# Kernel tuning notes

Measured on AMD Instinct MI355X. Metric: run time of the kernel, lower is better.

## Reference

```python
import jax, jax.numpy as jnp
import numpy as np

NUM_HEADS = 8
NUM_LEVELS = 4
NUM_POINTS = 4


def setup_inputs() -> dict:
    key = jax.random.key(0)
    kq, kp, kv, k1, k2, k3, k4 = jax.random.split(key, 7)
    B, Q, C = 4, 4096, 256
    M, L, P = NUM_HEADS, NUM_LEVELS, NUM_POINTS
    shapes_np = np.array([[128, 128], [64, 64], [32, 32], [16, 16]], dtype=np.int32)
    sizes = shapes_np[:, 0] * shapes_np[:, 1]
    N = int(sizes.sum())  # 21760
    level_index = jnp.asarray(np.concatenate([[0], np.cumsum(sizes)[:-1]]).astype(np.int32))
    q = jax.random.normal(kq, (B, Q, C), jnp.float32)
    p = jax.random.uniform(kp, (B, Q, L, 2), jnp.float32)  # normalized ref points
    v = jax.random.normal(kv, (B, N, C), jnp.float32)
    # proj_offset bias: radial grid init from reset_parameters()
    t = np.arange(M, dtype=np.float32) * (2.0 * np.pi / M)
    grid = np.stack([np.cos(t), np.sin(t)], -1)
    grid = grid / np.abs(grid).max(-1, keepdims=True)
    grid = np.tile(grid[:, None, None, :], (1, L, P, 1)) * np.arange(1, P + 1, dtype=np.float32)[None, None, :, None]
    b_off = jnp.asarray(grid.reshape(-1))
    s = 1.0 / np.sqrt(C).astype(np.float32)
    W_off = jax.random.normal(k1, (C, M * L * P * 2), jnp.float32) * 0.01
    W_attn = jax.random.normal(k2, (C, M * L * P), jnp.float32) * s
    b_attn = jnp.zeros((M * L * P,), jnp.float32)
    W_val = jax.random.normal(k3, (C, C), jnp.float32) * s
    b_val = jnp.zeros((C,), jnp.float32)
    W_out = jax.random.normal(k4, (C, C), jnp.float32) * s
    b_out = jnp.zeros((C,), jnp.float32)
    return {"q": q, "p": p, "v": v, "shapes": jnp.asarray(shapes_np), "level_index": level_index,
            "W_off": W_off, "b_off": b_off, "W_attn": W_attn, "b_attn": b_attn,
            "W_val": W_val, "b_val": b_val, "W_out": W_out, "b_out": b_out}


def _ms_deform_attn(q, p, v, shapes, level_index, W_off, b_off, W_attn, b_attn, W_val, b_val, W_out, b_out):
    B, Q, C = q.shape
    M, L, P = NUM_HEADS, NUM_LEVELS, NUM_POINTS
    D = C // M
    N = v.shape[1]
    # value projection -> [B, M, N, D] (head-major for gather)
    v_p = (v @ W_val + b_val).reshape(B, N, M, D).transpose(0, 2, 1, 3)
    # attention weights, softmax over L*P (classic MSDeformAttn kernel contract)
    attn = jax.nn.softmax((q @ W_attn + b_attn).reshape(B, Q, M, L * P), axis=-1)
    attn = attn.reshape(B, Q, M, L, P)
    # sampling locations (P==2 reference-point branch)
    off = (q @ W_off + b_off).reshape(B, Q, M, L, P, 2)
    norm = jnp.stack([shapes[:, 1], shapes[:, 0]], -1).astype(jnp.float32)  # (W, H) per level
    loc = p[:, :, None, :, None, :] + off / norm[None, None, None, :, None, :]  # [B,Q,M,L,P,2]

    out = jnp.zeros((B, M, Q, D), jnp.float32)
    for l in range(L):
        Hf = shapes[l, 0].astype(jnp.float32)
        Wf = shapes[l, 1].astype(jnp.float32)
        Hi = shapes[l, 0]
        Wi = shapes[l, 1]
        base = level_index[l]
        # grid_sample(align_corners=False) convention: pixel = loc*size - 0.5
        x = loc[:, :, :, l, :, 0] * Wf - 0.5  # [B,Q,M,P]
        y = loc[:, :, :, l, :, 1] * Hf - 0.5
        x0 = jnp.floor(x)
        y0 = jnp.floor(y)
        lx, ly = x - x0, y - y0
        x0i = x0.astype(jnp.int32)
        y0i = y0.astype(jnp.int32)

        def corner(xi, yi, w):
            valid = (xi >= 0) & (xi < Wi) & (yi >= 0) & (yi < Hi)
            idx = base + jnp.clip(yi, 0, Hi - 1) * Wi + jnp.clip(xi, 0, Wi - 1)  # [B,Q,M,P]
            idx = idx.transpose(0, 2, 1, 3).reshape(B, M, Q * P)
            g = jnp.take_along_axis(v_p, idx[..., None], axis=2).reshape(B, M, Q, P, D)
            wv = (w * valid.astype(w.dtype)).transpose(0, 2, 1, 3)[..., None]  # [B,M,Q,P,1]
            return g * wv

        samp = (corner(x0i, y0i, (1 - lx) * (1 - ly))
                + corner(x0i + 1, y0i, lx * (1 - ly))
                + corner(x0i, y0i + 1, (1 - lx) * ly)
                + corner(x0i + 1, y0i + 1, lx * ly))  # [B,M,Q,P,D]
        a_l = attn[:, :, :, l, :].transpose(0, 2, 1, 3)  # [B,M,Q,P]
        out = out + jnp.einsum('bmqpd,bmqp->bmqd', samp, a_l)

    out = out.transpose(0, 2, 1, 3).reshape(B, Q, M * D)
    return out @ W_out + b_out


def reference(q, p, v, shapes, level_index, W_off, b_off, W_attn, b_attn, W_val, b_val, W_out, b_out):
    return _ms_deform_attn(q, p, v, shapes, level_index, W_off, b_off, W_attn, b_attn, W_val, b_val, W_out, b_out)
```

## Files before the change

kernel.cpp:

```cpp
#include <hip/hip_runtime.h>
#include <cstddef>

#define BB 4
#define QQ 4096
#define MM 8
#define NN 21760

typedef __bf16 bf16_8 __attribute__((ext_vector_type(8)));
typedef __bf16 bf16_4 __attribute__((ext_vector_type(4)));
typedef float  floatx4 __attribute__((ext_vector_type(4)));

__global__ __launch_bounds__(256) void prep_weights(
    const float* __restrict__ Wv, const float* __restrict__ Wa,
    const float* __restrict__ Wo, const float* __restrict__ Wu,
    const float* __restrict__ ba, const float* __restrict__ bo,
    __bf16* __restrict__ Wt, float* __restrict__ biasq)
{
    const int gid = blockIdx.x * 256 + threadIdx.x;
    if (gid < 65536) {
        const int n = gid >> 8, k = gid & 255;
        Wt[gid] = (__bf16)Wv[k * 256 + n];
    } else if (gid < 163840) {
        const int o = gid - 65536;
        const int n = o >> 8, k = o & 255;
        Wt[gid] = (__bf16)(n < 128 ? Wa[k * 128 + n] : Wo[k * 256 + (n - 128)]);
    } else if (gid < 229376) {
        const int o = gid - 163840;
        const int n = o >> 8, k = o & 255;
        Wt[gid] = (__bf16)Wu[k * 256 + n];
    } else if (gid < 229760) {
        const int j = gid - 229376;
        biasq[j] = (j < 128) ? ba[j] : bo[j - 128];
    }
}

__global__ __launch_bounds__(512, 4) void gemm_vq(
    const float* __restrict__ v,
    const float* __restrict__ q,
    const __bf16* __restrict__ Wt,
    const float* __restrict__ b_val,
    const float* __restrict__ biasq,
    __bf16* __restrict__ vpb,
    float* __restrict__ gqp)
{
    __shared__ __bf16 As[64][256];

    const int tid  = threadIdx.x;
    const int lane = tid & 63;
    const int wave = tid >> 6;
    const int quad = lane >> 4;
    const int l16  = lane & 15;
    const int flat = blockIdx.x;

    if (flat >= 768) {
        const int f2     = flat - 768;
        const int z      = f2 / 340;
        const int token0 = (f2 - z * 340) * 64;
        const float* Af  = v + (size_t)z * NN * 256;

        #pragma unroll
        for (int c = 0; c < 8; ++c) {
            const int cid = c * 512 + tid;
            const int r   = cid >> 6;
            const int kc  = (cid & 63) * 4;
            const float4 av = *(const float4*)(Af + (size_t)(token0 + r) * 256 + kc);
            bf16_4 w;
            w[0] = (__bf16)av.x; w[1] = (__bf16)av.y;
            w[2] = (__bf16)av.z; w[3] = (__bf16)av.w;
            const int col = ((((kc >> 3) ^ (r & 7)) << 3) | (kc & 7));
            *(bf16_4*)&As[r][col] = w;
        }

        bf16_8 wf[8][2];
        #pragma unroll
        for (int kk = 0; kk < 8; ++kk)
            #pragma unroll
            for (int j = 0; j < 2; ++j)
                wf[kk][j] = *(const bf16_8*)(Wt + (size_t)(wave * 32 + j * 16 + l16) * 256
                                              + kk * 32 + quad * 8);
        __syncthreads();

        floatx4 acc[2][4] = {};
        #pragma unroll
        for (int kk = 0; kk < 8; ++kk) {
            bf16_8 af[4];
            #pragma unroll
            for (int it = 0; it < 4; ++it)
                af[it] = *(const bf16_8*)&As[it * 16 + l16]
                                           [(((kk * 4 + quad) ^ (l16 & 7)) << 3)];
            #pragma unroll
            for (int j = 0; j < 2; ++j)
                #pragma unroll
                for (int it = 0; it < 4; ++it)
                    acc[j][it] = __builtin_amdgcn_mfma_f32_16x16x32_bf16(wf[kk][j], af[it], acc[j][it], 0, 0, 0);
        }

        #pragma unroll
        for (int j = 0; j < 2; ++j) {
            const int n0 = wave * 32 + j * 16 + quad * 4;
            const float4 b4 = *(const float4*)(b_val + n0);
            const int mh = n0 >> 5, dd = n0 & 31;
            #pragma unroll
            for (int it = 0; it < 4; ++it) {
                const int token = token0 + it * 16 + l16;
                bf16_4 ob;
                ob[0] = (__bf16)(acc[j][it][0] + b4.x);
                ob[1] = (__bf16)(acc[j][it][1] + b4.y);
                ob[2] = (__bf16)(acc[j][it][2] + b4.z);
                ob[3] = (__bf16)(acc[j][it][3] + b4.w);
                *(bf16_4*)(vpb + (((size_t)z * 8 + mh) * NN + token) * 32 + dd) = ob;
            }
        }
    } else {
        const int o      = flat;
        const int slice  = o >> 8;
        const int token0 = (o & 255) * 64;
        const int col0   = slice * 128;
        const __bf16* Wb = Wt + 65536 + (size_t)col0 * 256;

        #pragma unroll
        for (int c = 0; c < 8; ++c) {
            const int cid = c * 512 + tid;
            const int r   = cid >> 6;
            const int kc  = (cid & 63) * 4;
            const float4 av = *(const float4*)(q + (size_t)(token0 + r) * 256 + kc);
            bf16_4 w;
            w[0] = (__bf16)av.x; w[1] = (__bf16)av.y;
            w[2] = (__bf16)av.z; w[3] = (__bf16)av.w;
            const int col = ((((kc >> 3) ^ (r & 7)) << 3) | (kc & 7));
            *(bf16_4*)&As[r][col] = w;
        }

        bf16_8 wf[8];
        #pragma unroll
        for (int kk = 0; kk < 8; ++kk)
            wf[kk] = *(const bf16_8*)(Wb + (size_t)(wave * 16 + l16) * 256
                                       + kk * 32 + quad * 8);
        __syncthreads();

        floatx4 acc[4] = {};
        #pragma unroll
        for (int kk = 0; kk < 8; ++kk) {
            bf16_8 af[4];
            #pragma unroll
            for (int it = 0; it < 4; ++it)
                af[it] = *(const bf16_8*)&As[it * 16 + l16]
                                           [(((kk * 4 + quad) ^ (l16 & 7)) << 3)];
            #pragma unroll
            for (int it = 0; it < 4; ++it)
                acc[it] = __builtin_amdgcn_mfma_f32_16x16x32_bf16(wf[kk], af[it], acc[it], 0, 0, 0);
        }

        const int n0 = col0 + wave * 16 + quad * 4;
        const float4 b4 = *(const float4*)(biasq + n0);
        #pragma unroll
        for (int it = 0; it < 4; ++it) {
            const int token = token0 + it * 16 + l16;
            float4 ot;
            ot.x = acc[it][0] + b4.x;
            ot.y = acc[it][1] + b4.y;
            ot.z = acc[it][2] + b4.z;
            ot.w = acc[it][3] + b4.w;
            *(float4*)(gqp + (size_t)token * 384 + n0) = ot;
        }
    }
}

__device__ __forceinline__ float bflo(unsigned u) { return __uint_as_float(u << 16); }
__device__ __forceinline__ float bfhi(unsigned u) { return __uint_as_float(u & 0xffff0000u); }

__global__ __launch_bounds__(512) void sampler_out(
    const __bf16* __restrict__ vp,
    const float* __restrict__ gqp,
    const float* __restrict__ pref,
    const __bf16* __restrict__ Wout,
    const float* __restrict__ b_out,
    float* __restrict__ out)
{
    __shared__ __bf16 mids[16][256];

    const int t    = threadIdx.x;
    const int m    = t >> 6;
    const int lane = t & 63;
    const int s    = lane >> 2;
    const int c    = lane & 3;
    const int l    = s >> 2;
    const int bq0  = blockIdx.x * 16;

    const int   Hi = 128 >> l;
    const float Hf = (float)Hi;
    const int   base = (l == 0) ? 0 : (l == 1) ? 16384 : (l == 2) ? 20480 : 21504;
    const int b2 = (lane >> 2) & 1, b3 = (lane >> 3) & 1, b4i = (lane >> 4) & 1;

    for (int qi = 0; qi < 16; ++qi) {
        const int bq = bq0 + qi;
        const int b  = bq >> 12;

        const float logit = gqp[(size_t)bq * 384 + m * 16 + s];
        const float e = __expf(logit);
        float sum = e;
        #pragma unroll
        for (int k = 4; k < 64; k <<= 1) sum += __shfl_xor(sum, k, 64);
        const float a = e * __builtin_amdgcn_rcpf(sum);

        const float2 off = *(const float2*)(gqp + (size_t)bq * 384 + 128 + (m * 16 + s) * 2);
        const float2 pr  = *(const float2*)(pref + (size_t)bq * 8 + l * 2);

        const float x = fmaf(pr.x, Hf, off.x - 0.5f);
        const float y = fmaf(pr.y, Hf, off.y - 0.5f);
        const float x0f = floorf(x), y0f = floorf(y);
        const float lx = x - x0f, ly = y - y0f;
        const int x0 = (int)x0f, y0 = (int)y0f;
        const int cx0 = min(max(x0, 0), Hi - 1), cx1 = min(max(x0 + 1, 0), Hi - 1);
        const int cy0 = min(max(y0, 0), Hi - 1), cy1 = min(max(y0 + 1, 0), Hi - 1);
        const bool vx0 = (x0 >= 0) && (x0 < Hi), vx1 = (x0 + 1 >= 0) && (x0 + 1 < Hi);
        const bool vy0 = (y0 >= 0) && (y0 < Hi), vy1 = (y0 + 1 >= 0) && (y0 + 1 < Hi);
        const float w00 = a * (1.f - lx) * (1.f - ly) * ((vx0 && vy0) ? 1.f : 0.f);
        const float w10 = a * lx * (1.f - ly) * ((vx1 && vy0) ? 1.f : 0.f);
        const float w01 = a * (1.f - lx) * ly * ((vx0 && vy1) ? 1.f : 0.f);
        const float w11 = a * lx * ly * ((vx1 && vy1) ? 1.f : 0.f);

        const __bf16* vbase = vp + ((size_t)b * 8 + m) * NN * 32;
        const uint4 u00 = *((const uint4*)(vbase + (size_t)(base + cy0 * Hi + cx0) * 32) + c);
        const uint4 u10 = *((const uint4*)(vbase + (size_t)(base + cy0 * Hi + cx1) * 32) + c);
        const uint4 u01 = *((const uint4*)(vbase + (size_t)(base + cy1 * Hi + cx0) * 32) + c);
        const uint4 u11 = *((const uint4*)(vbase + (size_t)(base + cy1 * Hi + cx1) * 32) + c);

        float f[8];
        f[0] = w00*bflo(u00.x) + w10*bflo(u10.x) + w01*bflo(u01.x) + w11*bflo(u11.x);
        f[1] = w00*bfhi(u00.x) + w10*bfhi(u10.x) + w01*bfhi(u01.x) + w11*bfhi(u11.x);
        f[2] = w00*bflo(u00.y) + w10*bflo(u10.y) + w01*bflo(u01.y) + w11*bflo(u11.y);
        f[3] = w00*bfhi(u00.y) + w10*bfhi(u10.y) + w01*bfhi(u01.y) + w11*bfhi(u11.y);
        f[4] = w00*bflo(u00.z) + w10*bflo(u10.z) + w01*bflo(u01.z) + w11*bflo(u11.z);
        f[5] = w00*bfhi(u00.z) + w10*bfhi(u10.z) + w01*bfhi(u01.z) + w11*bfhi(u11.z);
        f[6] = w00*bflo(u00.w) + w10*bflo(u10.w) + w01*bflo(u01.w) + w11*bflo(u11.w);
        f[7] = w00*bfhi(u00.w) + w10*bfhi(u10.w) + w01*bfhi(u01.w) + w11*bfhi(u11.w);

        #pragma unroll
        for (int j = 0; j < 4; ++j) {
            const float sel  = b2 ? f[j] : f[j + 4];
            const float recv = __shfl_xor(sel, 4, 64);
            f[j] = (b2 ? f[j + 4] : f[j]) + recv;
        }
        #pragma unroll
        for (int j = 0; j < 2; ++j) {
            const float sel  = b3 ? f[j] : f[j + 2];
            const float recv = __shfl_xor(sel, 8, 64);
            f[j] = (b3 ? f[j + 2] : f[j]) + recv;
        }
        {
            const float sel  = b4i ? f[0] : f[1];
            const float recv = __shfl_xor(sel, 16, 64);
            f[0] = (b4i ? f[1] : f[0]) + recv;
        }
        f[0] += __shfl_xor(f[0], 32, 64);

        if (!(lane & 32)) {
            const int chan = (c << 3) | (b2 << 2) | (b3 << 1) | b4i;
            const int cf   = m * 32 + chan;
            const int p = ((((cf >> 3) ^ (qi & 7)) << 3) | (cf & 7));
            mids[qi][p] = (__bf16)f[0];
        }
    }
    __syncthreads();

    const int quad = lane >> 4;
    const int l16  = lane & 15;

    bf16_8 wf[8][2];
    #pragma unroll
    for (int kk = 0; kk < 8; ++kk)
        #pragma unroll
        for (int j = 0; j < 2; ++j)
            wf[kk][j] = *(const bf16_8*)(Wout + (size_t)(m * 32 + j * 16 + l16) * 256
                                          + kk * 32 + quad * 8);

    floatx4 acc[2] = {};
    #pragma unroll
    for (int kk = 0; kk < 8; ++kk) {
        const bf16_8 af = *(const bf16_8*)&mids[l16][(((kk * 4 + quad) ^ (l16 & 7)) << 3)];
        #pragma unroll
        for (int j = 0; j < 2; ++j)
            acc[j] = __builtin_amdgcn_mfma_f32_16x16x32_bf16(wf[kk][j], af, acc[j], 0, 0, 0);
    }

    #pragma unroll
    for (int j = 0; j < 2; ++j) {
        const int n0 = m * 32 + j * 16 + quad * 4;
        const float4 b4 = *(const float4*)(b_out + n0);
        const int token = bq0 + l16;
        float4 o;
        o.x = acc[j][0] + b4.x;
        o.y = acc[j][1] + b4.y;
        o.z = acc[j][2] + b4.z;
        o.w = acc[j][3] + b4.w;
        *(float4*)(out + (size_t)token * 256 + n0) = o;
    }
}

extern "C" void kernel_launch(void* const* d_in, const int* in_sizes, int n_in,
                              void* d_out, int out_size, void* d_ws, size_t ws_size,
                              hipStream_t stream) {
    const float* q      = (const float*)d_in[0];
    const float* p      = (const float*)d_in[1];
    const float* v      = (const float*)d_in[2];
    const float* W_off  = (const float*)d_in[5];
    const float* b_off  = (const float*)d_in[6];
    const float* W_attn = (const float*)d_in[7];
    const float* b_attn = (const float*)d_in[8];
    const float* W_val  = (const float*)d_in[9];
    const float* b_val  = (const float*)d_in[10];
    const float* W_out  = (const float*)d_in[11];
    const float* b_out  = (const float*)d_in[12];
    float* out = (float*)d_out;

    float*  gqp   = (float*)d_ws;
    float*  biasq = gqp + (size_t)16384 * 384;
    __bf16* mid   = (__bf16*)(biasq + 384);
    __bf16* vpb   = mid + (size_t)16384 * 256;
    __bf16* Wt    = vpb + (size_t)BB * 8 * NN * 32;
    __bf16* Wt_out = Wt + 163840;

    prep_weights<<<898, 256, 0, stream>>>(W_val, W_attn, W_off, W_out, b_attn, b_off, Wt, biasq);

    gemm_vq<<<2128, 512, 0, stream>>>(v, q, Wt, b_val, biasq, vpb, gqp);

    sampler_out<<<1024, 512, 0, stream>>>(vpb, gqp, p, Wt_out, b_out, out);
}
```

Measured before the change: 261.9 us.

## Use 1024-thread blocks with 128-token tiles for value and query projections

The projection GEMM kernel now launches 1024-thread blocks. Value blocks cover 128 tokens, with each of 16 waves owning 16 output columns. Query blocks pack two independent 64-token jobs into the two halves of the block. The value-tile load also batches its global float4 loads before converting to bf16, to expose more memory parallelism. Block count is halved and each block uses twice the shared memory, which may reduce occupancy per CU and change tail behaviour.

Result: no change. 261.7 us (-0.1%).

```diff
diff --git a/kernel.cpp b/kernel.cpp
--- a/kernel.cpp
+++ b/kernel.cpp
@@ -34,7 +34,7 @@
     }
 }
 
-__global__ __launch_bounds__(512, 4) void gemm_vq(
+__global__ __launch_bounds__(1024, 4) void gemm_vpq(
     const float* __restrict__ v,
     const float* __restrict__ q,
     const __bf16* __restrict__ Wt,
@@ -43,112 +43,115 @@
     __bf16* __restrict__ vpb,
     float* __restrict__ gqp)
 {
-    __shared__ __bf16 As[64][256];
+    __shared__ __bf16 As[128][256];
 
     const int tid  = threadIdx.x;
     const int lane = tid & 63;
-    const int wave = tid >> 6;
     const int quad = lane >> 4;
     const int l16  = lane & 15;
     const int flat = blockIdx.x;
 
-    if (flat >= 768) {
-        const int f2     = flat - 768;
-        const int z      = f2 / 340;
-        const int token0 = (f2 - z * 340) * 64;
+    if (flat < 680) {
+        const int z      = flat / 170;
+        const int token0 = (flat - z * 170) * 128;
         const float* Af  = v + (size_t)z * NN * 256;
+        const int w      = tid >> 6;
+
+        bf16_8 wf[8];
+        #pragma unroll
+        for (int kk = 0; kk < 8; ++kk)
+            wf[kk] = *(const bf16_8*)(Wt + (size_t)(w * 16 + l16) * 256
+                                       + kk * 32 + quad * 8);
+
+        #pragma unroll
+        for (int h = 0; h < 2; ++h) {
+            float4 a4[4];
+            #pragma unroll
+            for (int c = 0; c < 4; ++c) {
+                const int cid = (h * 4 + c) * 1024 + tid;
+                const int r   = cid >> 6;
+                const int kc  = (cid & 63) * 4;
+                a4[c] = *(const float4*)(Af + (size_t)(token0 + r) * 256 + kc);
+            }
+            #pragma unroll
+            for (int c = 0; c < 4; ++c) {
+                const int cid = (h * 4 + c) * 1024 + tid;
+                const int r   = cid >> 6;
+                const int kc  = (cid & 63) * 4;
+                bf16_4 wv;
+                wv[0] = (__bf16)a4[c].x; wv[1] = (__bf16)a4[c].y;
+                wv[2] = (__bf16)a4[c].z; wv[3] = (__bf16)a4[c].w;
+                const int col = ((((kc >> 3) ^ (r & 7)) << 3) | (kc & 7));
+                *(bf16_4*)&As[r][col] = wv;
+            }
+        }
+        __syncthreads();
+
+        floatx4 acc[8] = {};
+        #pragma unroll
+        for (int kk = 0; kk < 8; ++kk) {
+            #pragma unroll
+            for (int it = 0; it < 8; ++it) {
+                const bf16_8 af = *(const bf16_8*)&As[it * 16 + l16]
+                                      [(((kk * 4 + quad) ^ (l16 & 7)) << 3)];
+                acc[it] = __builtin_amdgcn_mfma_f32_16x16x32_bf16(wf[kk], af, acc[it], 0, 0, 0);
+            }
+        }
+
+        const int n0 = w * 16 + quad * 4;
+        const float4 b4 = *(const float4*)(b_val + n0);
+        const int mh = n0 >> 5, dd = n0 & 31;
+        #pragma unroll
+        for (int it = 0; it < 8; ++it) {
+            const int token = token0 + it * 16 + l16;
+            bf16_4 ob;
+            ob[0] = (__bf16)(acc[it][0] + b4.x);
+            ob[1] = (__bf16)(acc[it][1] + b4.y);
+            ob[2] = (__bf16)(acc[it][2] + b4.z);
+            ob[3] = (__bf16)(acc[it][3] + b4.w);
+            *(bf16_4*)(vpb + (((size_t)z * 8 + mh) * NN + token) * 32 + dd) = ob;
+        }
+    } else {
+        const int o     = flat - 680;
+        const int hw    = tid >> 9;
+        const int t5    = tid & 511;
+        const int wave  = t5 >> 6;
+        const int job   = o * 2 + hw;
+        const int slice = job >> 8;
+        const int token0 = (job & 255) * 64;
+        const int col0   = slice * 128;
+        const int rbase  = hw * 64;
+        const __bf16* Wb = Wt + 65536 + (size_t)col0 * 256;
+
+        bf16_8 wf[8];
+        #pragma unroll
+        for (int kk = 0; kk < 8; ++kk)
+            wf[kk] = *(const bf16_8*)(Wb + (size_t)(wave * 16 + l16) * 256
+                                       + kk * 32 + quad * 8);
 
         #pragma unroll
         for (int c = 0; c < 8; ++c) {
-            const int cid = c * 512 + tid;
-            const int r   = cid >> 6;
-            const int kc  = (cid & 63) * 4;
-            const float4 av = *(const float4*)(Af + (size_t)(token0 + r) * 256 + kc);
-            bf16_4 w;
-            w[0] = (__bf16)av.x; w[1] = (__bf16)av.y;
-            w[2] = (__bf16)av.z; w[3] = (__bf16)av.w;
-            const int col = ((((kc >> 3) ^ (r & 7)) << 3) | (kc & 7));
-            *(bf16_4*)&As[r][col] = w;
-        }
-
-        bf16_8 wf[8][2];
-        #pragma unroll
-        for (int kk = 0; kk < 8; ++kk)
-            #pragma unroll
-            for (int j = 0; j < 2; ++j)
-                wf[kk][j] = *(const bf16_8*)(Wt + (size_t)(wave * 32 + j * 16 + l16) * 256
-                                              + kk * 32 + quad * 8);
-        __syncthreads();
-
-        floatx4 acc[2][4] = {};
-        #pragma unroll
-        for (int kk = 0; kk < 8; ++kk) {
-            bf16_8 af[4];
-            #pragma unroll
-            for (int it = 0; it < 4; ++it)
-                af[it] = *(const bf16_8*)&As[it * 16 + l16]
-                                           [(((kk * 4 + quad) ^ (l16 & 7)) << 3)];
-            #pragma unroll
-            for (int j = 0; j < 2; ++j)
-                #pragma unroll
-                for (int it = 0; it < 4; ++it)
-                    acc[j][it] = __builtin_amdgcn_mfma_f32_16x16x32_bf16(wf[kk][j], af[it], acc[j][it], 0, 0, 0);
-        }
-
-        #pragma unroll
-        for (int j = 0; j < 2; ++j) {
-            const int n0 = wave * 32 + j * 16 + quad * 4;
-            const float4 b4 = *(const float4*)(b_val + n0);
-            const int mh = n0 >> 5, dd = n0 & 31;
-            #pragma unroll
-            for (int it = 0; it < 4; ++it) {
-                const int token = token0 + it * 16 + l16;
-                bf16_4 ob;
-                ob[0] = (__bf16)(acc[j][it][0] + b4.x);
-                ob[1] = (__bf16)(acc[j][it][1] + b4.y);
-                ob[2] = (__bf16)(acc[j][it][2] + b4.z);
-                ob[3] = (__bf16)(acc[j][it][3] + b4.w);
-                *(bf16_4*)(vpb + (((size_t)z * 8 + mh) * NN + token) * 32 + dd) = ob;
-            }
-        }
-    } else {
-        const int o      = flat;
-        const int slice  = o >> 8;
-        const int token0 = (o & 255) * 64;
-        const int col0   = slice * 128;
-        const __bf16* Wb = Wt + 65536 + (size_t)col0 * 256;
-
-        #pragma unroll
-        for (int c = 0; c < 8; ++c) {
-            const int cid = c * 512 + tid;
+            const int cid = c * 512 + t5;
             const int r   = cid >> 6;
             const int kc  = (cid & 63) * 4;
             const float4 av = *(const float4*)(q + (size_t)(token0 + r) * 256 + kc);
-            bf16_4 w;
-            w[0] = (__bf16)av.x; w[1] = (__bf16)av.y;
-            w[2] = (__bf16)av.z; w[3] = (__bf16)av.w;
+            bf16_4 wv;
+            wv[0] = (__bf16)av.x; wv[1] = (__bf16)av.y;
+            wv[2] = (__bf16)av.z; wv[3] = (__bf16)av.w;
             const int col = ((((kc >> 3) ^ (r & 7)) << 3) | (kc & 7));
-            *(bf16_4*)&As[r][col] = w;
-        }
-
-        bf16_8 wf[8];
-        #pragma unroll
-        for (int kk = 0; kk < 8; ++kk)
-            wf[kk] = *(const bf16_8*)(Wb + (size_t)(wave * 16 + l16) * 256
-                                       + kk * 32 + quad * 8);
+            *(bf16_4*)&As[rbase + r][col] = wv;
+        }
         __syncthreads();
 
         floatx4 acc[4] = {};
         #pragma unroll
         for (int kk = 0; kk < 8; ++kk) {
-            bf16_8 af[4];
             #pragma unroll
-            for (int it = 0; it < 4; ++it)
-                af[it] = *(const bf16_8*)&As[it * 16 + l16]
-                                           [(((kk * 4 + quad) ^ (l16 & 7)) << 3)];
-            #pragma unroll
-            for (int it = 0; it < 4; ++it)
-                acc[it] = __builtin_amdgcn_mfma_f32_16x16x32_bf16(wf[kk], af[it], acc[it], 0, 0, 0);
+            for (int it = 0; it < 4; ++it) {
+                const bf16_8 af = *(const bf16_8*)&As[rbase + it * 16 + l16]
+                                      [(((kk * 4 + quad) ^ (l16 & 7)) << 3)];
+                acc[it] = __builtin_amdgcn_mfma_f32_16x16x32_bf16(wf[kk], af, acc[it], 0, 0, 0);
+            }
         }
 
         const int n0 = col0 + wave * 16 + quad * 4;
@@ -323,7 +326,7 @@
 
     prep_weights<<<898, 256, 0, stream>>>(W_val, W_attn, W_off, W_out, b_attn, b_off, Wt, biasq);
 
-    gemm_vq<<<2128, 512, 0, stream>>>(v, q, Wt, b_val, biasq, vpb, gqp);
+    gemm_vpq<<<1064, 1024, 0, stream>>>(v, q, Wt, b_val, biasq, vpb, gqp);
 
     sampler_out<<<1024, 512, 0, stream>>>(vpb, gqp, p, Wt_out, b_out, out);
 }
```

## Pre-swizzle weights into MFMA fragment order and restructure projection GEMM tiling

Applied to the files above, without the earlier changes.

Weights are now stored in MFMA fragment order, so each lane fetches a contiguous bf16x8 straight from global memory. The fp32 activations are also loaded and converted directly into registers, which removes the LDS staging and its barrier before the MFMA loop. Each wave computes a 32-token by 64-column tile. The value-projection output is staged through swizzled LDS so it can be written to the head-major layout with wide, coalesced stores, and the grid shrinks accordingly. In exchange, activation loads from global are less coalesced, and each block rereads the weights from cache.

Measured after the change: 287.0 us. 1.1x slower.

```diff
diff --git a/kernel.cpp b/kernel.cpp
--- a/kernel.cpp
+++ b/kernel.cpp
@@ -9,6 +9,10 @@
 typedef __bf16 bf16_8 __attribute__((ext_vector_type(8)));
 typedef __bf16 bf16_4 __attribute__((ext_vector_type(4)));
 typedef float  floatx4 __attribute__((ext_vector_type(4)));
+
+__host__ __device__ __forceinline__ int fragoff(int n, int k) {
+    return (((n >> 4) * 8 + (k >> 5)) * 4 + ((k >> 3) & 3)) * 128 + ((n & 15) * 8) + (k & 7);
+}
 
 __global__ __launch_bounds__(256) void prep_weights(
     const float* __restrict__ Wv, const float* __restrict__ Wa,
@@ -19,22 +23,23 @@
     const int gid = blockIdx.x * 256 + threadIdx.x;
     if (gid < 65536) {
         const int n = gid >> 8, k = gid & 255;
-        Wt[gid] = (__bf16)Wv[k * 256 + n];
+        Wt[fragoff(n, k)] = (__bf16)Wv[k * 256 + n];
     } else if (gid < 163840) {
         const int o = gid - 65536;
         const int n = o >> 8, k = o & 255;
-        Wt[gid] = (__bf16)(n < 128 ? Wa[k * 128 + n] : Wo[k * 256 + (n - 128)]);
+        Wt[65536 + fragoff(n, k)] =
+            (__bf16)(n < 128 ? Wa[k * 128 + n] : Wo[k * 256 + (n - 128)]);
     } else if (gid < 229376) {
         const int o = gid - 163840;
         const int n = o >> 8, k = o & 255;
-        Wt[gid] = (__bf16)Wu[k * 256 + n];
+        Wt[163840 + o] = (__bf16)Wu[k * 256 + n];
     } else if (gid < 229760) {
         const int j = gid - 229376;
         biasq[j] = (j < 128) ? ba[j] : bo[j - 128];
     }
 }
 
-__global__ __launch_bounds__(512, 4) void gemm_vq(
+__global__ __launch_bounds__(512, 4) void gemm_vs(
     const float* __restrict__ v,
     const float* __restrict__ q,
     const __bf16* __restrict__ Wt,
@@ -43,7 +48,7 @@
     __bf16* __restrict__ vpb,
     float* __restrict__ gqp)
 {
-    __shared__ __bf16 As[64][256];
+    __shared__ __bf16 Ts[64][256];
 
     const int tid  = threadIdx.x;
     const int lane = tid & 63;
@@ -52,116 +57,128 @@
     const int l16  = lane & 15;
     const int flat = blockIdx.x;
 
-    if (flat >= 768) {
-        const int f2     = flat - 768;
-        const int z      = f2 / 340;
-        const int token0 = (f2 - z * 340) * 64;
-        const float* Af  = v + (size_t)z * NN * 256;
-
-        #pragma unroll
-        for (int c = 0; c < 8; ++c) {
-            const int cid = c * 512 + tid;
-            const int r   = cid >> 6;
-            const int kc  = (cid & 63) * 4;
-            const float4 av = *(const float4*)(Af + (size_t)(token0 + r) * 256 + kc);
-            bf16_4 w;
-            w[0] = (__bf16)av.x; w[1] = (__bf16)av.y;
-            w[2] = (__bf16)av.z; w[3] = (__bf16)av.w;
-            const int col = ((((kc >> 3) ^ (r & 7)) << 3) | (kc & 7));
-            *(bf16_4*)&As[r][col] = w;
-        }
-
-        bf16_8 wf[8][2];
-        #pragma unroll
-        for (int kk = 0; kk < 8; ++kk)
-            #pragma unroll
-            for (int j = 0; j < 2; ++j)
-                wf[kk][j] = *(const bf16_8*)(Wt + (size_t)(wave * 32 + j * 16 + l16) * 256
-                                              + kk * 32 + quad * 8);
+    if (flat < 1360) {
+        const int z      = flat / 340;
+        const int tok0   = (flat - z * 340) * 64;
+        const int colgrp = wave & 3;
+        const int tokgrp = wave >> 2;
+        const int tok_base = tok0 + tokgrp * 32;
+        const float* A0 = v + (size_t)z * NN * 256 + (size_t)(tok_base + l16) * 256;
+
+        floatx4 acc[2][4] = {};
+        #pragma unroll 2
+        for (int kk = 0; kk < 8; ++kk) {
+            bf16_8 wb[4];
+            #pragma unroll
+            for (int j = 0; j < 4; ++j) {
+                const int nf = colgrp * 4 + j;
+                wb[j] = *(const bf16_8*)(Wt + ((nf * 8 + kk) * 4 + quad) * 128 + l16 * 8);
+            }
+            bf16_8 fa[2];
+            #pragma unroll
+            for (int it = 0; it < 2; ++it) {
+                const float* ap = A0 + it * 16 * 256 + kk * 32 + quad * 8;
+                const float4 x0 = *(const float4*)ap;
+                const float4 x1 = *(const float4*)(ap + 4);
+                bf16_8 t;
+                t[0] = (__bf16)x0.x; t[1] = (__bf16)x0.y;
+                t[2] = (__bf16)x0.z; t[3] = (__bf16)x0.w;
+                t[4] = (__bf16)x1.x; t[5] = (__bf16)x1.y;
+                t[6] = (__bf16)x1.z; t[7] = (__bf16)x1.w;
+                fa[it] = t;
+            }
+            #pragma unroll
+            for (int it = 0; it < 2; ++it)
+                #pragma unroll
+                for (int j = 0; j < 4; ++j)
+                    acc[it][j] = __builtin_amdgcn_mfma_f32_16x16x32_bf16(wb[j], fa[it], acc[it][j], 0, 0, 0);
+        }
+
+        #pragma unroll
+        for (int j = 0; j < 4; ++j) {
+            const int n0  = colgrp * 64 + j * 16 + quad * 4;
+            const int blk = n0 >> 3;
+            const float4 b4 = *(const float4*)(b_val + n0);
+            #pragma unroll
+            for (int it = 0; it < 2; ++it) {
+                const int tok = tokgrp * 32 + it * 16 + l16;
+                bf16_4 ob;
+                ob[0] = (__bf16)(acc[it][j][0] + b4.x);
+                ob[1] = (__bf16)(acc[it][j][1] + b4.y);
+                ob[2] = (__bf16)(acc[it][j][2] + b4.z);
+                ob[3] = (__bf16)(acc[it][j][3] + b4.w);
+                *(bf16_4*)&Ts[tok][((blk ^ (tok & 7)) << 3) | (n0 & 7)] = ob;
+            }
+        }
         __syncthreads();
 
+        const int head = tid >> 6;
+        const size_t runbase = (((size_t)z * 8 + head) * NN + tok0) * 32;
+        #pragma unroll
+        for (int c = 0; c < 4; ++c) {
+            const int tok = c * 16 + (lane >> 2);
+            const int cb  = head * 4 + (lane & 3);
+            const bf16_8 val = *(const bf16_8*)&Ts[tok][((cb ^ (tok & 7)) << 3)];
+            *(bf16_8*)(vpb + runbase + c * 512 + lane * 8) = val;
+        }
+    } else {
+        int tok_base, colbase;
+        if (flat < 1616) {
+            const int idx = flat - 1360;
+            colbase  = (wave & 3) * 64;
+            tok_base = idx * 64 + (wave >> 2) * 32;
+        } else {
+            const int idx = flat - 1616;
+            colbase  = 256 + (wave & 1) * 64;
+            tok_base = idx * 128 + (wave >> 1) * 32;
+        }
+        const float* A0 = q + (size_t)(tok_base + l16) * 256;
+        const __bf16* Wq = Wt + 65536;
+        const int nfbase = colbase >> 4;
+
         floatx4 acc[2][4] = {};
-        #pragma unroll
+        #pragma unroll 2
         for (int kk = 0; kk < 8; ++kk) {
-            bf16_8 af[4];
-            #pragma unroll
-            for (int it = 0; it < 4; ++it)
-                af[it] = *(const bf16_8*)&As[it * 16 + l16]
-                                           [(((kk * 4 + quad) ^ (l16 & 7)) << 3)];
-            #pragma unroll
-            for (int j = 0; j < 2; ++j)
+            bf16_8 wb[4];
+            #pragma unroll
+            for (int j = 0; j < 4; ++j) {
+                const int nf = nfbase + j;
+                wb[j] = *(const bf16_8*)(Wq + ((nf * 8 + kk) * 4 + quad) * 128 + l16 * 8);
+            }
+            bf16_8 fa[2];
+            #pragma unroll
+            for (int it = 0; it < 2; ++it) {
+                const float* ap = A0 + it * 16 * 256 + kk * 32 + quad * 8;
+                const float4 x0 = *(const float4*)ap;
+                const float4 x1 = *(const float4*)(ap + 4);
+                bf16_8 t;
+                t[0] = (__bf16)x0.x; t[1] = (__bf16)x0.y;
+                t[2] = (__bf16)x0.z; t[3] = (__bf16)x0.w;
+                t[4] = (__bf16)x1.x; t[5] = (__bf16)x1.y;
+                t[6] = (__bf16)x1.z; t[7] = (__bf16)x1.w;
+                fa[it] = t;
+            }
+            #pragma unroll
+            for (int it = 0; it < 2; ++it)
                 #pragma unroll
-                for (int it = 0; it < 4; ++it)
-                    acc[j][it] = __builtin_amdgcn_mfma_f32_16x16x32_bf16(wf[kk][j], af[it], acc[j][it], 0, 0, 0);
-        }
-
-        #pragma unroll
-        for (int j = 0; j < 2; ++j) {
-            const int n0 = wave * 32 + j * 16 + quad * 4;
-            const float4 b4 = *(const float4*)(b_val + n0);
-            const int mh = n0 >> 5, dd = n0 & 31;
-            #pragma unroll
-            for (int it = 0; it < 4; ++it) {
-                const int token = token0 + it * 16 + l16;
-                bf16_4 ob;
-                ob[0] = (__bf16)(acc[j][it][0] + b4.x);
-                ob[1] = (__bf16)(acc[j][it][1] + b4.y);
-                ob[2] = (__bf16)(acc[j][it][2] + b4.z);
-                ob[3] = (__bf16)(acc[j][it][3] + b4.w);
-                *(bf16_4*)(vpb + (((size_t)z * 8 + mh) * NN + token) * 32 + dd) = ob;
-            }
-        }
-    } else {
-        const int o      = flat;
-        const int slice  = o >> 8;
-        const int token0 = (o & 255) * 64;
-        const int col0   = slice * 128;
-        const __bf16* Wb = Wt + 65536 + (size_t)col0 * 256;
-
-        #pragma unroll
-        for (int c = 0; c < 8; ++c) {
-            const int cid = c * 512 + tid;
-            const int r   = cid >> 6;
-            const int kc  = (cid & 63) * 4;
-            const float4 av = *(const float4*)(q + (size_t)(token0 + r) * 256 + kc);
-            bf16_4 w;
-            w[0] = (__bf16)av.x; w[1] = (__bf16)av.y;
-            w[2] = (__bf16)av.z; w[3] = (__bf16)av.w;
-            const int col = ((((kc >> 3) ^ (r & 7)) << 3) | (kc & 7));
-            *(bf16_4*)&As[r][col] = w;
-        }
-
-        bf16_8 wf[8];
-        #pragma unroll
-        for (int kk = 0; kk < 8; ++kk)
-            wf[kk] = *(const bf16_8*)(Wb + (size_t)(wave * 16 + l16) * 256
-                                       + kk * 32 + quad * 8);
-        __syncthreads();
-
-        floatx4 acc[4] = {};
-        #pragma unroll
-        for (int kk = 0; kk < 8; ++kk) {
-            bf16_8 af[4];
-            #pragma unroll
-            for (int it = 0; it < 4; ++it)
-                af[it] = *(const bf16_8*)&As[it * 16 + l16]
-                                           [(((kk * 4 + quad) ^ (l16 & 7)) << 3)];
-            #pragma unroll
-            for (int it = 0; it < 4; ++it)
-                acc[it] = __builtin_amdgcn_mfma_f32_16x16x32_bf16(wf[kk], af[it], acc[it], 0, 0, 0);
-        }
-
-        const int n0 = col0 + wave * 16 + quad * 4;
-        const float4 b4 = *(const float4*)(biasq + n0);
-        #pragma unroll
-        for (int it = 0; it < 4; ++it) {
-            const int token = token0 + it * 16 + l16;
-            float4 ot;
-            ot.x = acc[it][0] + b4.x;
-            ot.y = acc[it][1] + b4.y;
-            ot.z = acc[it][2] + b4.z;
-            ot.w = acc[it][3] + b4.w;
-            *(float4*)(gqp + (size_t)token * 384 + n0) = ot;
+                for (int j = 0; j < 4; ++j)
+                    acc[it][j] = __builtin_amdgcn_mfma_f32_16x16x32_bf16(wb[j], fa[it], acc[it][j], 0, 0, 0);
+        }
+
+        #pragma unroll
+        for (int j = 0; j < 4; ++j) {
+            const int n0 = colbase + j * 16 + quad * 4;
+            const float4 b4 = *(const float4*)(biasq + n0);
+            #pragma unroll
+            for (int it = 0; it < 2; ++it) {
+                const int token = tok_base + it * 16 + l16;
+                float4 ot;
+                ot.x = acc[it][j][0] + b4.x;
+                ot.y = acc[it][j][1] + b4.y;
+                ot.z = acc[it][j][2] + b4.z;
+                ot.w = acc[it][j][3] + b4.w;
+                *(float4*)(gqp + (size_t)token * 384 + n0) = ot;
+            }
         }
     }
 }
@@ -323,7 +340,7 @@
 
     prep_weights<<<898, 256, 0, stream>>>(W_val, W_attn, W_off, W_out, b_attn, b_off, Wt, biasq);
 
-    gemm_vq<<<2128, 512, 0, stream>>>(v, q, Wt, b_val, biasq, vpb, gqp);
+    gemm_vs<<<1744, 512, 0, stream>>>(v, q, Wt, b_val, biasq, vpb, gqp);
 
     sampler_out<<<1024, 512, 0, stream>>>(vpb, gqp, p, Wt_out, b_out, out);
 }
```
